# Optimization experiments

Measured on AMD Instinct MI355X. Metric: run time of the kernel, lower is better.

## Reference

```python
import jax, jax.numpy as jnp
import numpy as np

GROUP_SIZE = 128
HIDDEN = 2048
INTER = 5632
TOKENS = 8192
_SHIFTS = jnp.arange(8, dtype=jnp.uint32) * 4  # 4-bit nibbles, 8 per int32


def _pack_rows(nib):
    # nib: [in, out] int values in [0,16); pack 8 consecutive rows into one int32
    r, c = nib.shape
    n = nib.reshape(r // 8, 8, c).astype(jnp.uint32)
    packed = jnp.sum(n << _SHIFTS[None, :, None], axis=1, dtype=jnp.uint32)
    return jax.lax.bitcast_convert_type(packed, jnp.int32)  # [in//8, out]


def _pack_cols(nib):
    # nib: [groups, out]; pack 8 consecutive cols into one int32
    g, o = nib.shape
    n = nib.reshape(g, o // 8, 8).astype(jnp.uint32)
    packed = jnp.sum(n << _SHIFTS[None, None, :], axis=-1, dtype=jnp.uint32)
    return jax.lax.bitcast_convert_type(packed, jnp.int32)  # [groups, out//8]


def _dequant(qweight, qzeros, scales, group_size=GROUP_SIZE):
    # GPTQ int4 dequant: w = (q - (z + 1)) * scale, per group of `group_size` input rows
    in_packed, out = qweight.shape
    in_dim = in_packed * 8
    groups = scales.shape[0]
    sh = jnp.arange(8, dtype=jnp.int32) * 4
    q = (qweight[:, None, :] >> sh[None, :, None]) & 0xF       # [in//8, 8, out]
    q = q.reshape(in_dim, out)
    z = (qzeros[:, :, None] >> sh[None, None, :]) & 0xF        # [groups, out//8, 8]
    z = z.reshape(groups, out)
    gidx = jnp.arange(in_dim) // group_size                    # [in]
    w = (q - (z[gidx] + 1)).astype(scales.dtype) * scales[gidx]
    return w  # [in, out]


def setup_inputs() -> dict:
    key = jax.random.key(0)
    ks = jax.random.split(key, 10)
    x = jax.random.normal(ks[0], (TOKENS, HIDDEN), dtype=jnp.float32)

    def make(kq, kz, ksc, in_dim, out_dim):
        qn = jax.random.randint(kq, (in_dim, out_dim), 0, 16, dtype=jnp.int32)
        zn = jax.random.randint(kz, (in_dim // GROUP_SIZE, out_dim), 0, 16, dtype=jnp.int32)
        sc = jax.random.uniform(ksc, (in_dim // GROUP_SIZE, out_dim), jnp.float32, 1e-3, 2e-2)
        return _pack_rows(qn), _pack_cols(zn), sc

    gq, gz, gs = make(ks[1], ks[2], ks[3], HIDDEN, INTER)
    uq, uz, us = make(ks[4], ks[5], ks[6], HIDDEN, INTER)
    dq, dz, ds = make(ks[7], ks[8], ks[9], INTER, HIDDEN)
    return {
        "x": x,
        "gate_qweight": gq, "gate_qzeros": gz, "gate_scales": gs,
        "up_qweight": uq, "up_qzeros": uz, "up_scales": us,
        "down_qweight": dq, "down_qzeros": dz, "down_scales": ds,
    }


def reference(x, gate_qweight, gate_qzeros, gate_scales,
              up_qweight, up_qzeros, up_scales,
              down_qweight, down_qzeros, down_scales):
    wg = _dequant(gate_qweight, gate_qzeros, gate_scales)  # [H, I]
    wu = _dequant(up_qweight, up_qzeros, up_scales)        # [H, I]
    wd = _dequant(down_qweight, down_qzeros, down_scales)  # [I, H]
    # fused_gate_up: silu(x @ Wg) * (x @ Wu)
    h = jax.nn.silu(x @ wg) * (x @ wu)                     # [T, I]
    return h @ wd                                          # [T, H]
```

## Files before the change

### kernel.cpp

```cpp
#include <hip/hip_runtime.h>

#define TOKENS 8192
#define HIDDEN 2048
#define INTER  5632

typedef _Float16 f16x8 __attribute__((ext_vector_type(8)));
typedef float    f32x4 __attribute__((ext_vector_type(4)));

__device__ __forceinline__ void async_copy16(const void* g, void* l) {
  __builtin_amdgcn_global_load_lds(
      (const __attribute__((address_space(1))) unsigned int*)g,
      (__attribute__((address_space(3))) unsigned int*)l, 16, 0, 0);
}

#define BAR   __builtin_amdgcn_s_barrier()
#define SB0   __builtin_amdgcn_sched_barrier(0)
#define LGKM0 do { asm volatile("s_waitcnt lgkmcnt(0)" ::: "memory"); SB0; } while (0)
#define WAITVM(n) asm volatile("s_waitcnt vmcnt(" #n ")" ::: "memory")
#define PRIO(x) __builtin_amdgcn_s_setprio(x)


__global__ void k_convert_x(const float* __restrict__ x, _Float16* __restrict__ xs) {
  const int kb = blockIdx.x;
  const int mt = blockIdx.y;
  const int m  = threadIdx.x;
  const float* src = x + (size_t)(mt * 128 + m) * HIDDEN + kb * 8;
  float4 f0 = *(const float4*)src;
  float4 f1 = *(const float4*)(src + 4);
  f16x8 v;
  v[0] = (_Float16)f0.x; v[1] = (_Float16)f0.y; v[2] = (_Float16)f0.z; v[3] = (_Float16)f0.w;
  v[4] = (_Float16)f1.x; v[5] = (_Float16)f1.y; v[6] = (_Float16)f1.z; v[7] = (_Float16)f1.w;
  *(f16x8*)(xs + ((size_t)(mt * 256 + kb) * 128 + m) * 8) = v;
}

__global__ void k_dequant(const unsigned int* __restrict__ qw,
                          const unsigned int* __restrict__ qz,
                          const float* __restrict__ sc,
                          _Float16* __restrict__ out, int N, int N8) {
  const int n  = blockIdx.x * 256 + threadIdx.x;
  const int k8 = blockIdx.y;
  const int g  = k8 >> 4;
  unsigned int q  = qw[(size_t)k8 * N + n];
  unsigned int zw = qz[(size_t)g * N8 + (n >> 3)];
  int   z1 = (int)((zw >> ((n & 7) * 4)) & 0xFu) + 1;
  float s  = sc[(size_t)g * N + n];
  f16x8 w;
#pragma unroll
  for (int j = 0; j < 8; ++j)
    w[j] = (_Float16)((float)((int)((q >> (4 * j)) & 0xFu) - z1) * s);
  *(f16x8*)(out + ((size_t)k8 * N + n) * 8) = w;
}

__global__ __launch_bounds__(512, 1)
void k_gemm_gateup(const _Float16* __restrict__ xs,
                   const _Float16* __restrict__ wg,
                   const _Float16* __restrict__ wu,
                   _Float16* __restrict__ hs) {
  extern __shared__ _Float16 lds[];
  _Float16* A0  = lds;
  _Float16* A1  = lds + 16384;
  _Float16* Bg0 = lds + 32768;
  _Float16* Bg1 = lds + 40960;
  _Float16* Bu0 = lds + 49152;
  _Float16* Bu1 = lds + 57344;

  const int bid  = blockIdx.x;
  const int wgid = (bid & 7) * 176 + (bid >> 3);
  const int mt = wgid / 44, nt = wgid % 44;

  const int tid  = threadIdx.x;
  const int wave = tid >> 6, lane = tid & 63;
  const int wm = wave >> 1, wn = wave & 1;
  const int row16 = lane >> 4, col = lane & 15;

  int afo[4], bfo[4];
#pragma unroll
  for (int i = 0; i < 4; ++i) {
    afo[i] = (wm >> 1) * 8192 + row16 * 1024 + ((wm & 1) * 64 + i * 16 + col) * 8;
    bfo[i] = row16 * 1024 + (wn * 64 + i * 16 + col) * 8;
  }

  const f32x4 zero = {0.f, 0.f, 0.f, 0.f};
  f32x4 accg[4][4], accu[4][4];
#pragma unroll
  for (int i = 0; i < 4; ++i)
#pragma unroll
    for (int j = 0; j < 4; ++j) { accg[i][j] = zero; accu[i][j] = zero; }

  f16x8 af[4][2], bf[2][2];

#define GU_LOAD_A(AP) \
  _Pragma("unroll") for (int mi_ = 0; mi_ < 4; ++mi_) \
  _Pragma("unroll") for (int ks_ = 0; ks_ < 2; ++ks_) \
    af[mi_][ks_] = *(const f16x8*)((AP) + afo[mi_] + ks_ * 4096);

#define GU_LOAD_B(BP, nh) \
  _Pragma("unroll") for (int ni_ = 0; ni_ < 2; ++ni_) \
  _Pragma("unroll") for (int ks_ = 0; ks_ < 2; ++ks_) \
    bf[ni_][ks_] = *(const f16x8*)((BP) + bfo[(nh) * 2 + ni_] + ks_ * 4096);

#define GU_MFMA(ACC, nh) \
  _Pragma("unroll") for (int mi_ = 0; mi_ < 4; ++mi_) \
  _Pragma("unroll") for (int ni_ = 0; ni_ < 2; ++ni_) \
  _Pragma("unroll") for (int ks_ = 0; ks_ < 2; ++ks_) \
    ACC[mi_][(nh) * 2 + ni_] = __builtin_amdgcn_mfma_f32_16x16x32_f16( \
        af[mi_][ks_], bf[ni_][ks_], ACC[mi_][(nh) * 2 + ni_], 0, 0, 0);

#define GU_STAGE_A(AP, kt) do { const int kt_ = (kt); \
  _Pragma("unroll") for (int q_ = 0; q_ < 4; ++q_) { \
    const int i_ = q_ * 512 + tid; \
    async_copy16(xs + (size_t)(((2 * mt + (i_ >> 10)) * 256 + kt_ * 8 + ((i_ >> 7) & 7)) * 128 + (i_ & 127)) * 8, \
                 (char*)(AP) + q_ * 8192 + wave * 1024); } } while (0)

#define GU_STAGE_B(BP, W, kt) do { const int kt_ = (kt); \
  _Pragma("unroll") for (int q_ = 0; q_ < 2; ++q_) { \
    const int i_ = q_ * 512 + tid; \
    async_copy16((W) + (size_t)((kt_ * 8 + (i_ >> 7)) * INTER + nt * 128 + (i_ & 127)) * 8, \
                 (char*)(BP) + q_ * 8192 + wave * 1024); } } while (0)

  GU_STAGE_A(A0, 0); GU_STAGE_B(Bg0, wg, 0); GU_STAGE_B(Bu0, wu, 0);
  GU_STAGE_A(A1, 1); GU_STAGE_B(Bg1, wg, 1);
  WAITVM(6);
  BAR; SB0;

  for (int t2 = 0; t2 < 16; ++t2) {
    const int O  = 2 * t2 + 1;
    const int e2 = (2 * t2 + 2 < 32) ? 2 * t2 + 2 : 31;
    const int o2 = (2 * t2 + 3 < 32) ? 2 * t2 + 3 : 31;
    GU_LOAD_A(A0); GU_LOAD_B(Bg0, 0); GU_STAGE_B(Bu1, wu, O);
    BAR; LGKM0; PRIO(1); GU_MFMA(accg, 0); PRIO(0); BAR; SB0;
    GU_LOAD_B(Bg0, 1); GU_STAGE_A(A0, e2);
    BAR; LGKM0; PRIO(1); GU_MFMA(accg, 1); PRIO(0); BAR; SB0;
    GU_LOAD_B(Bu0, 0); GU_STAGE_B(Bg0, wg, e2);
    BAR; LGKM0; PRIO(1); GU_MFMA(accu, 0); PRIO(0); BAR; SB0;
    GU_LOAD_B(Bu0, 1);
    BAR; LGKM0; PRIO(1); GU_MFMA(accu, 1); PRIO(0); WAITVM(6); BAR; SB0;
    GU_LOAD_A(A1); GU_LOAD_B(Bg1, 0); GU_STAGE_B(Bu0, wu, e2);
    BAR; LGKM0; PRIO(1); GU_MFMA(accg, 0); PRIO(0); BAR; SB0;
    GU_LOAD_B(Bg1, 1); GU_STAGE_A(A1, o2);
    BAR; LGKM0; PRIO(1); GU_MFMA(accg, 1); PRIO(0); BAR; SB0;
    GU_LOAD_B(Bu1, 0); GU_STAGE_B(Bg1, wg, o2);
    BAR; LGKM0; PRIO(1); GU_MFMA(accu, 0); PRIO(0); BAR; SB0;
    GU_LOAD_B(Bu1, 1);
    BAR; LGKM0; PRIO(1); GU_MFMA(accu, 1); PRIO(0); WAITVM(6); BAR; SB0;
  }
  WAITVM(0);

  const size_t mt128 = (size_t)(2 * mt + (wm >> 1));
#pragma unroll
  for (int mi = 0; mi < 4; ++mi)
#pragma unroll
    for (int ni = 0; ni < 4; ++ni) {
      const int kg = nt * 128 + wn * 64 + ni * 16 + col;
      const size_t base = (mt128 * 704 + (size_t)(kg >> 3)) * 1024 + (kg & 7);
#pragma unroll
      for (int r = 0; r < 4; ++r) {
        const float g = accg[mi][ni][r], u = accu[mi][ni][r];
        const float h = g / (1.f + __expf(-g)) * u;
        const int mloc = (wm & 1) * 64 + mi * 16 + row16 * 4 + r;
        hs[base + (size_t)mloc * 8] = (_Float16)h;
      }
    }
#undef GU_LOAD_A
#undef GU_LOAD_B
#undef GU_MFMA
#undef GU_STAGE_A
#undef GU_STAGE_B
}

__global__ __launch_bounds__(512, 1)
void k_gemm_down(const _Float16* __restrict__ hs,
                 const _Float16* __restrict__ wd,
                 float* __restrict__ out) {
  extern __shared__ _Float16 lds[];
  _Float16* A0 = lds;
  _Float16* A1 = lds + 16384;
  _Float16* B0 = lds + 32768;
  _Float16* B1 = lds + 49152;

  const int bid  = blockIdx.x;
  const int wgid = (bid & 7) * 32 + (bid >> 3);
  const int nt = wgid >> 5, mt = wgid & 31;

  const int tid  = threadIdx.x;
  const int wave = tid >> 6, lane = tid & 63;
  const int wm = wave >> 2, wn = wave & 3;
  const int row16 = lane >> 4, col = lane & 15;

  int afo[8], bfo[4];
#pragma unroll
  for (int i = 0; i < 8; ++i)
    afo[i] = wm * 8192 + row16 * 1024 + (i * 16 + col) * 8;
#pragma unroll
  for (int i = 0; i < 4; ++i)
    bfo[i] = row16 * 2048 + (wn * 64 + i * 16 + col) * 8;

  const f32x4 zero = {0.f, 0.f, 0.f, 0.f};
  f32x4 acc[8][4];
#pragma unroll
  for (int i = 0; i < 8; ++i)
#pragma unroll
    for (int j = 0; j < 4; ++j) acc[i][j] = zero;

  f16x8 af[4][2], bf[4][2];

#define DN_LOAD_A(AP, mh) \
  _Pragma("unroll") for (int mi_ = 0; mi_ < 4; ++mi_) \
  _Pragma("unroll") for (int ks_ = 0; ks_ < 2; ++ks_) \
    af[mi_][ks_] = *(const f16x8*)((AP) + afo[(mh) * 4 + mi_] + ks_ * 4096);

#define DN_LOAD_B(BP, nh) \
  _Pragma("unroll") for (int ni_ = 0; ni_ < 2; ++ni_) \
  _Pragma("unroll") for (int ks_ = 0; ks_ < 2; ++ks_) \
    bf[(nh) * 2 + ni_][ks_] = *(const f16x8*)((BP) + bfo[(nh) * 2 + ni_] + ks_ * 8192);

#define DN_MFMA(mh, nh) \
  _Pragma("unroll") for (int mi_ = 0; mi_ < 4; ++mi_) \
  _Pragma("unroll") for (int ni_ = 0; ni_ < 2; ++ni_) \
  _Pragma("unroll") for (int ks_ = 0; ks_ < 2; ++ks_) \
    acc[(mh) * 4 + mi_][(nh) * 2 + ni_] = __builtin_amdgcn_mfma_f32_16x16x32_f16( \
        af[mi_][ks_], bf[(nh) * 2 + ni_][ks_], acc[(mh) * 4 + mi_][(nh) * 2 + ni_], 0, 0, 0);

#define DN_STAGE_A(AP, kt) do { const int kt_ = (kt); \
  _Pragma("unroll") for (int q_ = 0; q_ < 4; ++q_) { \
    const int i_ = q_ * 512 + tid; \
    async_copy16(hs + (size_t)(((2 * mt + (i_ >> 10)) * 704 + kt_ * 8 + ((i_ >> 7) & 7)) * 128 + (i_ & 127)) * 8, \
                 (char*)(AP) + q_ * 8192 + wave * 1024); } } while (0)

#define DN_STAGE_B(BP, kt) do { const int kt_ = (kt); \
  _Pragma("unroll") for (int q_ = 0; q_ < 4; ++q_) { \
    const int i_ = q_ * 512 + tid; \
    async_copy16(wd + (size_t)((kt_ * 8 + (i_ >> 8)) * HIDDEN + nt * 256 + (i_ & 255)) * 8, \
                 (char*)(BP) + q_ * 8192 + wave * 1024); } } while (0)

  DN_STAGE_B(B0, 0); DN_STAGE_A(A0, 0);
  DN_STAGE_B(B1, 1); DN_STAGE_A(A1, 1);
  WAITVM(8);
  BAR; SB0;

  for (int t2 = 0; t2 < 44; ++t2) {
    const int e2 = (2 * t2 + 2 < 88) ? 2 * t2 + 2 : 87;
    const int o2 = (2 * t2 + 3 < 88) ? 2 * t2 + 3 : 87;
    DN_LOAD_A(A0, 0); DN_LOAD_B(B0, 0);
    BAR; LGKM0; PRIO(1); DN_MFMA(0, 0); PRIO(0); BAR; SB0;
    DN_LOAD_B(B0, 1);
    BAR; LGKM0; PRIO(1); DN_MFMA(0, 1); PRIO(0); BAR; SB0;
    DN_LOAD_A(A0, 1); DN_STAGE_B(B0, e2);
    BAR; LGKM0; PRIO(1); DN_MFMA(1, 0); PRIO(0); BAR; SB0;
    DN_STAGE_A(A0, e2);
    BAR; LGKM0; PRIO(1); DN_MFMA(1, 1); PRIO(0); WAITVM(8); BAR; SB0;
    DN_LOAD_A(A1, 0); DN_LOAD_B(B1, 0);
    BAR; LGKM0; PRIO(1); DN_MFMA(0, 0); PRIO(0); BAR; SB0;
    DN_LOAD_B(B1, 1);
    BAR; LGKM0; PRIO(1); DN_MFMA(0, 1); PRIO(0); BAR; SB0;
    DN_LOAD_A(A1, 1); DN_STAGE_B(B1, o2);
    BAR; LGKM0; PRIO(1); DN_MFMA(1, 0); PRIO(0); BAR; SB0;
    DN_STAGE_A(A1, o2);
    BAR; LGKM0; PRIO(1); DN_MFMA(1, 1); PRIO(0); WAITVM(8); BAR; SB0;
  }
  WAITVM(0);

#pragma unroll
  for (int mi = 0; mi < 8; ++mi)
#pragma unroll
    for (int ni = 0; ni < 4; ++ni) {
      const int n = nt * 256 + wn * 64 + ni * 16 + col;
#pragma unroll
      for (int r = 0; r < 4; ++r) {
        const int m = mt * 256 + wm * 128 + mi * 16 + row16 * 4 + r;
        out[(size_t)m * HIDDEN + n] = acc[mi][ni][r];
      }
    }
#undef DN_LOAD_A
#undef DN_LOAD_B
#undef DN_MFMA
#undef DN_STAGE_A
#undef DN_STAGE_B
}

extern "C" void kernel_launch(void* const* d_in, const int* in_sizes, int n_in,
                              void* d_out, int out_size, void* d_ws, size_t ws_size,
                              hipStream_t stream) {
  (void)in_sizes; (void)n_in; (void)out_size; (void)ws_size;
  const float*        x  = (const float*)d_in[0];
  const unsigned int* gq = (const unsigned int*)d_in[1];
  const unsigned int* gz = (const unsigned int*)d_in[2];
  const float*        gs = (const float*)d_in[3];
  const unsigned int* uq = (const unsigned int*)d_in[4];
  const unsigned int* uz = (const unsigned int*)d_in[5];
  const float*        us = (const float*)d_in[6];
  const unsigned int* dq = (const unsigned int*)d_in[7];
  const unsigned int* dz = (const unsigned int*)d_in[8];
  const float*        ds = (const float*)d_in[9];
  float* out = (float*)d_out;

  char* ws = (char*)d_ws;
  _Float16* xs  = (_Float16*)ws;
  _Float16* wgd = (_Float16*)(ws + (size_t)TOKENS * HIDDEN * 2);
  _Float16* wud = wgd + (size_t)HIDDEN * INTER;
  _Float16* wdd = wud + (size_t)HIDDEN * INTER;
  _Float16* hs  = wdd + (size_t)INTER * HIDDEN;

  static bool attr_set = false;
  if (!attr_set) {
    hipFuncSetAttribute((const void*)k_gemm_gateup,
                        hipFuncAttributeMaxDynamicSharedMemorySize, 131072);
    hipFuncSetAttribute((const void*)k_gemm_down,
                        hipFuncAttributeMaxDynamicSharedMemorySize, 131072);
    attr_set = true;
  }

  k_convert_x<<<dim3(HIDDEN / 8, TOKENS / 128), 128, 0, stream>>>(x, xs);
  k_dequant<<<dim3(INTER / 256, HIDDEN / 8), 256, 0, stream>>>(gq, gz, gs, wgd, INTER, INTER / 8);
  k_dequant<<<dim3(INTER / 256, HIDDEN / 8), 256, 0, stream>>>(uq, uz, us, wud, INTER, INTER / 8);
  k_dequant<<<dim3(HIDDEN / 256, INTER / 8), 256, 0, stream>>>(dq, dz, ds, wdd, HIDDEN, HIDDEN / 8);
  k_gemm_gateup<<<dim3(1408), 512, 131072, stream>>>(xs, wgd, wud, hs);
  k_gemm_down<<<dim3(256), 512, 131072, stream>>>(hs, wdd, out);
}
```

Measured before the change: 708.7 us.

## Interleave gate and up weights into one B tile and combine via LDS epilogue

The gate/up GEMM now stages gate and up weight columns side by side in a single 256-wide B tile. Each wave computes a 128x64 slice, so waves with wn>=2 hold up results while waves with wn<2 hold gate results. The up accumulators are exchanged through LDS in the epilogue so SiLU(g)*u can be applied. This changes the wave tiling so each A fragment load feeds MFMAs over a wider N, cutting A-fragment LDS reads. It also rearranges the blockIdx-to-tile mapping, and in exchange adds an LDS round trip and extra barriers in the epilogue.

```diff
diff --git a/kernel.cpp b/kernel.cpp
--- a/kernel.cpp
+++ b/kernel.cpp
@@ -57,54 +57,53 @@
                    const _Float16* __restrict__ wu,
                    _Float16* __restrict__ hs) {
   extern __shared__ _Float16 lds[];
-  _Float16* A0  = lds;
-  _Float16* A1  = lds + 16384;
-  _Float16* Bg0 = lds + 32768;
-  _Float16* Bg1 = lds + 40960;
-  _Float16* Bu0 = lds + 49152;
-  _Float16* Bu1 = lds + 57344;
+  _Float16* A0 = lds;
+  _Float16* A1 = lds + 16384;
+  _Float16* B0 = lds + 32768;
+  _Float16* B1 = lds + 49152;
 
   const int bid  = blockIdx.x;
   const int wgid = (bid & 7) * 176 + (bid >> 3);
-  const int mt = wgid / 44, nt = wgid % 44;
+  const int nt = wgid >> 5, mt = wgid & 31;
 
   const int tid  = threadIdx.x;
   const int wave = tid >> 6, lane = tid & 63;
-  const int wm = wave >> 1, wn = wave & 1;
+  const int wm = wave >> 2, wn = wave & 3;
   const int row16 = lane >> 4, col = lane & 15;
 
-  int afo[4], bfo[4];
-#pragma unroll
-  for (int i = 0; i < 4; ++i) {
-    afo[i] = (wm >> 1) * 8192 + row16 * 1024 + ((wm & 1) * 64 + i * 16 + col) * 8;
-    bfo[i] = row16 * 1024 + (wn * 64 + i * 16 + col) * 8;
-  }
+  int afo[8], bfo[4];
+#pragma unroll
+  for (int i = 0; i < 8; ++i)
+    afo[i] = wm * 8192 + row16 * 1024 + (i * 16 + col) * 8;
+#pragma unroll
+  for (int i = 0; i < 4; ++i)
+    bfo[i] = row16 * 2048 + (wn * 64 + i * 16 + col) * 8;
 
   const f32x4 zero = {0.f, 0.f, 0.f, 0.f};
-  f32x4 accg[4][4], accu[4][4];
-#pragma unroll
-  for (int i = 0; i < 4; ++i)
-#pragma unroll
-    for (int j = 0; j < 4; ++j) { accg[i][j] = zero; accu[i][j] = zero; }
-
-  f16x8 af[4][2], bf[2][2];
-
-#define GU_LOAD_A(AP) \
+  f32x4 acc[8][4];
+#pragma unroll
+  for (int i = 0; i < 8; ++i)
+#pragma unroll
+    for (int j = 0; j < 4; ++j) acc[i][j] = zero;
+
+  f16x8 af[4][2], bf[4][2];
+
+#define GU_LOAD_A(AP, mh) \
   _Pragma("unroll") for (int mi_ = 0; mi_ < 4; ++mi_) \
   _Pragma("unroll") for (int ks_ = 0; ks_ < 2; ++ks_) \
-    af[mi_][ks_] = *(const f16x8*)((AP) + afo[mi_] + ks_ * 4096);
+    af[mi_][ks_] = *(const f16x8*)((AP) + afo[(mh) * 4 + mi_] + ks_ * 4096);
 
 #define GU_LOAD_B(BP, nh) \
   _Pragma("unroll") for (int ni_ = 0; ni_ < 2; ++ni_) \
   _Pragma("unroll") for (int ks_ = 0; ks_ < 2; ++ks_) \
-    bf[ni_][ks_] = *(const f16x8*)((BP) + bfo[(nh) * 2 + ni_] + ks_ * 4096);
-
-#define GU_MFMA(ACC, nh) \
+    bf[(nh) * 2 + ni_][ks_] = *(const f16x8*)((BP) + bfo[(nh) * 2 + ni_] + ks_ * 8192);
+
+#define GU_MFMA(mh, nh) \
   _Pragma("unroll") for (int mi_ = 0; mi_ < 4; ++mi_) \
   _Pragma("unroll") for (int ni_ = 0; ni_ < 2; ++ni_) \
   _Pragma("unroll") for (int ks_ = 0; ks_ < 2; ++ks_) \
-    ACC[mi_][(nh) * 2 + ni_] = __builtin_amdgcn_mfma_f32_16x16x32_f16( \
-        af[mi_][ks_], bf[ni_][ks_], ACC[mi_][(nh) * 2 + ni_], 0, 0, 0);
+    acc[(mh) * 4 + mi_][(nh) * 2 + ni_] = __builtin_amdgcn_mfma_f32_16x16x32_f16( \
+        af[mi_][ks_], bf[(nh) * 2 + ni_][ks_], acc[(mh) * 4 + mi_][(nh) * 2 + ni_], 0, 0, 0);
 
 #define GU_STAGE_A(AP, kt) do { const int kt_ = (kt); \
   _Pragma("unroll") for (int q_ = 0; q_ < 4; ++q_) { \
@@ -112,55 +111,73 @@
     async_copy16(xs + (size_t)(((2 * mt + (i_ >> 10)) * 256 + kt_ * 8 + ((i_ >> 7) & 7)) * 128 + (i_ & 127)) * 8, \
                  (char*)(AP) + q_ * 8192 + wave * 1024); } } while (0)
 
-#define GU_STAGE_B(BP, W, kt) do { const int kt_ = (kt); \
-  _Pragma("unroll") for (int q_ = 0; q_ < 2; ++q_) { \
+#define GU_STAGE_B(BP, kt) do { const int kt_ = (kt); \
+  _Pragma("unroll") for (int q_ = 0; q_ < 4; ++q_) { \
     const int i_ = q_ * 512 + tid; \
-    async_copy16((W) + (size_t)((kt_ * 8 + (i_ >> 7)) * INTER + nt * 128 + (i_ & 127)) * 8, \
+    const int kb_ = i_ >> 8, c_ = i_ & 255; \
+    const _Float16* bsrc_ = (c_ & 128) ? wu : wg; \
+    async_copy16(bsrc_ + (size_t)((kt_ * 8 + kb_) * INTER + nt * 128 + (c_ & 127)) * 8, \
                  (char*)(BP) + q_ * 8192 + wave * 1024); } } while (0)
 
-  GU_STAGE_A(A0, 0); GU_STAGE_B(Bg0, wg, 0); GU_STAGE_B(Bu0, wu, 0);
-  GU_STAGE_A(A1, 1); GU_STAGE_B(Bg1, wg, 1);
-  WAITVM(6);
+  GU_STAGE_B(B0, 0); GU_STAGE_A(A0, 0);
+  GU_STAGE_B(B1, 1); GU_STAGE_A(A1, 1);
+  WAITVM(8);
   BAR; SB0;
 
   for (int t2 = 0; t2 < 16; ++t2) {
-    const int O  = 2 * t2 + 1;
     const int e2 = (2 * t2 + 2 < 32) ? 2 * t2 + 2 : 31;
     const int o2 = (2 * t2 + 3 < 32) ? 2 * t2 + 3 : 31;
-    GU_LOAD_A(A0); GU_LOAD_B(Bg0, 0); GU_STAGE_B(Bu1, wu, O);
-    BAR; LGKM0; PRIO(1); GU_MFMA(accg, 0); PRIO(0); BAR; SB0;
-    GU_LOAD_B(Bg0, 1); GU_STAGE_A(A0, e2);
-    BAR; LGKM0; PRIO(1); GU_MFMA(accg, 1); PRIO(0); BAR; SB0;
-    GU_LOAD_B(Bu0, 0); GU_STAGE_B(Bg0, wg, e2);
-    BAR; LGKM0; PRIO(1); GU_MFMA(accu, 0); PRIO(0); BAR; SB0;
-    GU_LOAD_B(Bu0, 1);
-    BAR; LGKM0; PRIO(1); GU_MFMA(accu, 1); PRIO(0); WAITVM(6); BAR; SB0;
-    GU_LOAD_A(A1); GU_LOAD_B(Bg1, 0); GU_STAGE_B(Bu0, wu, e2);
-    BAR; LGKM0; PRIO(1); GU_MFMA(accg, 0); PRIO(0); BAR; SB0;
-    GU_LOAD_B(Bg1, 1); GU_STAGE_A(A1, o2);
-    BAR; LGKM0; PRIO(1); GU_MFMA(accg, 1); PRIO(0); BAR; SB0;
-    GU_LOAD_B(Bu1, 0); GU_STAGE_B(Bg1, wg, o2);
-    BAR; LGKM0; PRIO(1); GU_MFMA(accu, 0); PRIO(0); BAR; SB0;
-    GU_LOAD_B(Bu1, 1);
-    BAR; LGKM0; PRIO(1); GU_MFMA(accu, 1); PRIO(0); WAITVM(6); BAR; SB0;
+    GU_LOAD_A(A0, 0); GU_LOAD_B(B0, 0);
+    BAR; LGKM0; PRIO(1); GU_MFMA(0, 0); PRIO(0); BAR; SB0;
+    GU_LOAD_B(B0, 1);
+    BAR; LGKM0; PRIO(1); GU_MFMA(0, 1); PRIO(0); BAR; SB0;
+    GU_LOAD_A(A0, 1); GU_STAGE_B(B0, e2);
+    BAR; LGKM0; PRIO(1); GU_MFMA(1, 0); PRIO(0); BAR; SB0;
+    GU_STAGE_A(A0, e2);
+    BAR; LGKM0; PRIO(1); GU_MFMA(1, 1); PRIO(0); WAITVM(8); BAR; SB0;
+    GU_LOAD_A(A1, 0); GU_LOAD_B(B1, 0);
+    BAR; LGKM0; PRIO(1); GU_MFMA(0, 0); PRIO(0); BAR; SB0;
+    GU_LOAD_B(B1, 1);
+    BAR; LGKM0; PRIO(1); GU_MFMA(0, 1); PRIO(0); BAR; SB0;
+    GU_LOAD_A(A1, 1); GU_STAGE_B(B1, o2);
+    BAR; LGKM0; PRIO(1); GU_MFMA(1, 0); PRIO(0); BAR; SB0;
+    GU_STAGE_A(A1, o2);
+    BAR; LGKM0; PRIO(1); GU_MFMA(1, 1); PRIO(0); WAITVM(8); BAR; SB0;
   }
   WAITVM(0);
-
-  const size_t mt128 = (size_t)(2 * mt + (wm >> 1));
-#pragma unroll
-  for (int mi = 0; mi < 4; ++mi)
-#pragma unroll
-    for (int ni = 0; ni < 4; ++ni) {
-      const int kg = nt * 128 + wn * 64 + ni * 16 + col;
-      const size_t base = (mt128 * 704 + (size_t)(kg >> 3)) * 1024 + (kg & 7);
-#pragma unroll
-      for (int r = 0; r < 4; ++r) {
-        const float g = accg[mi][ni][r], u = accu[mi][ni][r];
-        const float h = g / (1.f + __expf(-g)) * u;
-        const int mloc = (wm & 1) * 64 + mi * 16 + row16 * 4 + r;
-        hs[base + (size_t)mloc * 8] = (_Float16)h;
-      }
+  __syncthreads();
+
+  {
+    float* xls = (float*)lds;
+    const int pairIdx = wm * 2 + (wn & 1);
+    if (wn >= 2) {
+      float* dst = xls + (size_t)pairIdx * 8192 + lane * 4;
+#pragma unroll
+      for (int mi = 0; mi < 8; ++mi)
+#pragma unroll
+        for (int ni = 0; ni < 4; ++ni)
+          *(f32x4*)(dst + (mi * 4 + ni) * 256) = acc[mi][ni];
     }
+    __syncthreads();
+    if (wn < 2) {
+      const float* srcp = xls + (size_t)pairIdx * 8192 + lane * 4;
+#pragma unroll
+      for (int mi = 0; mi < 8; ++mi)
+#pragma unroll
+        for (int ni = 0; ni < 4; ++ni) {
+          const f32x4 uv = *(const f32x4*)(srcp + (mi * 4 + ni) * 256);
+          const int kg = nt * 128 + wn * 64 + ni * 16 + col;
+          const size_t base = ((size_t)(mt * 2 + wm) * 704 + (kg >> 3)) * 1024 + (kg & 7);
+#pragma unroll
+          for (int r = 0; r < 4; ++r) {
+            const float g = acc[mi][ni][r];
+            const float h = g / (1.f + __expf(-g)) * uv[r];
+            const int mloc = mi * 16 + row16 * 4 + r;
+            hs[base + (size_t)mloc * 8] = (_Float16)h;
+          }
+        }
+    }
+  }
 #undef GU_LOAD_A
 #undef GU_LOAD_B
 #undef GU_MFMA
```

Result: no change. 718.6 us (+1.4%).
